# Kernel optimization log

Hardware: AMD Instinct MI355X
Metric: run time of the kernel (lower is better)

## Reference

```python
import jax, jax.numpy as jnp
import numpy as np

B, S, D, H, F, V = 64, 100, 1024, 16, 4096, 32000
DEPTH = D // H
EPS = 1e-6


def _positional_encoding(seq_len, dim):
    pos = np.arange(seq_len).reshape(seq_len, 1).astype(np.float64)
    i = np.arange(dim)
    div_term = np.power(10000.0, 2 * (i // 2) / dim)
    pe = np.zeros((seq_len, dim))
    pe[:, 0::2] = np.sin(pos / div_term[0::2])
    pe[:, 1::2] = np.cos(pos / div_term[1::2])
    return jnp.asarray(pe, dtype=jnp.float32)


def _layer_norm(x, gamma, beta):
    mean = jnp.mean(x, axis=-1, keepdims=True)
    var = jnp.mean(jnp.square(x - mean), axis=-1, keepdims=True)
    return gamma * ((x - mean) / jnp.sqrt(var + EPS)) + beta


def setup_inputs() -> dict:
    key = jax.random.key(0)
    ks = jax.random.split(key, 16)
    sd = 0.02
    inp = {
        "tokens": jax.random.randint(ks[0], (B, S), 0, V, dtype=jnp.int32),
        "emb_table": jax.random.normal(ks[1], (V, D), jnp.float32) * sd,
        "Wq": jax.random.normal(ks[2], (H, D, DEPTH), jnp.float32) * sd,
        "bq": jnp.zeros((H, DEPTH), jnp.float32),
        "Wk": jax.random.normal(ks[3], (H, D, DEPTH), jnp.float32) * sd,
        "bk": jnp.zeros((H, DEPTH), jnp.float32),
        "Wv": jax.random.normal(ks[4], (H, D, DEPTH), jnp.float32) * sd,
        "bv": jnp.zeros((H, DEPTH), jnp.float32),
        "Wo": jax.random.normal(ks[5], (D, D), jnp.float32) * sd,
        "bo": jnp.zeros((D,), jnp.float32),
        "W1": jax.random.normal(ks[6], (D, F), jnp.float32) * sd,
        "b1": jnp.zeros((F,), jnp.float32),
        "W2": jax.random.normal(ks[7], (F, D), jnp.float32) * sd,
        "b2": jnp.zeros((D,), jnp.float32),
        "gamma1": jnp.ones((D,), jnp.float32),
        "beta1": jnp.zeros((D,), jnp.float32),
        "gamma2": jnp.ones((D,), jnp.float32),
        "beta2": jnp.zeros((D,), jnp.float32),
    }
    return inp


def reference(tokens, emb_table, Wq, bq, Wk, bk, Wv, bv, Wo, bo,
              W1, b1, W2, b2, gamma1, beta1, gamma2, beta2):
    pe = _positional_encoding(S, D)  # [S, D]
    x = emb_table[tokens] + pe  # [B, S, D]

    # per-head projections (equivalent to the H separate Dense layers, stacked)
    q = jnp.einsum("bsd,hde->bhse", x, Wq) + bq[None, :, None, :]
    k = jnp.einsum("bsd,hde->bhse", x, Wk) + bk[None, :, None, :]
    v = jnp.einsum("bsd,hde->bhse", x, Wv) + bv[None, :, None, :]

    scores = jnp.einsum("bhqe,bhke->bhqk", q, k) / jnp.sqrt(jnp.float32(DEPTH))
    attn = jax.nn.softmax(scores, axis=-1)  # no mask (mask=False in Encoder)
    ctx = jnp.einsum("bhqk,bhke->bhqe", attn, v)  # [B, H, S, depth]
    # concat heads along last dim (head i -> columns i*depth:(i+1)*depth)
    ctx = jnp.transpose(ctx, (0, 2, 1, 3)).reshape(B, S, D)
    att_out = ctx @ Wo + bo

    # dropout is identity (training=False)
    x1 = _layer_norm(att_out + x, gamma1, beta1)
    ff = jax.nn.relu(x1 @ W1 + b1) @ W2 + b2
    out = _layer_norm(ff + x1, gamma2, beta2)
    return out
```

## Files before the change

kernel.cpp:

```cpp
#include <hip/hip_runtime.h>
#include <hip/hip_bf16.h>
#include <math.h>

typedef __hip_bfloat16 bf16;
typedef __attribute__((ext_vector_type(8))) short short8;
typedef __attribute__((ext_vector_type(4))) float f32x4;

static constexpr int kB = 64;
static constexpr int kS = 100;
static constexpr int kD = 1024;
static constexpr int kH = 16;
static constexpr int kF = 4096;
static constexpr int kRows = kB * kS;

__device__ __forceinline__ void gload_lds16(const void* g, void* l) {
    __builtin_amdgcn_global_load_lds(
        (const __attribute__((address_space(1))) void*)g,
        (__attribute__((address_space(3))) void*)l, 16, 0, 0);
}

union BF4 { bf16 b[4]; uint2 u; };

__global__ void pe_kernel(float* __restrict__ pe) {
    int idx = blockIdx.x * 256 + threadIdx.x;
    if (idx >= kS * kD) return;
    int s = idx / kD, i = idx % kD;
    double dt = pow(10000.0, (double)(2 * (i / 2)) / (double)kD);
    double a  = (double)s / dt;
    pe[idx] = (float)((i & 1) ? cos(a) : sin(a));
}

__global__ __launch_bounds__(256) void embed_kernel(
    const int* __restrict__ tokens, const float* __restrict__ emb,
    const float* __restrict__ pe, float* __restrict__ xf, bf16* __restrict__ xb) {
    int row = blockIdx.x, t = threadIdx.x;
    int tok = tokens[row];
    const float4* ev = (const float4*)(emb + (size_t)tok * kD);
    const float4* pv = (const float4*)(pe + (size_t)(row % kS) * kD);
    float4 a = ev[t], b = pv[t];
    float4 v; v.x = a.x + b.x; v.y = a.y + b.y; v.z = a.z + b.z; v.w = a.w + b.w;
    ((float4*)(xf + (size_t)row * kD))[t] = v;
    BF4 p; p.b[0] = __float2bfloat16(v.x); p.b[1] = __float2bfloat16(v.y);
    p.b[2] = __float2bfloat16(v.z); p.b[3] = __float2bfloat16(v.w);
    *(uint2*)(xb + (size_t)row * kD + t * 4) = p.u;
}

__global__ __launch_bounds__(256) void transpose_to_bf16(
    const float* __restrict__ in, bf16* __restrict__ out, int K, int N) {
    __shared__ float tile[64][65];
    size_t zoff = (size_t)blockIdx.z * K * N;
    int k0 = blockIdx.y * 64, n0 = blockIdx.x * 64;
    int t = threadIdx.x, r = t >> 6, c = t & 63;
#pragma unroll
    for (int it = 0; it < 16; ++it)
        tile[it * 4 + r][c] = in[zoff + (size_t)(k0 + it * 4 + r) * N + n0 + c];
    __syncthreads();
#pragma unroll
    for (int it = 0; it < 16; ++it)
        out[zoff + (size_t)(n0 + it * 4 + r) * K + k0 + c] =
            __float2bfloat16(tile[c][it * 4 + r]);
}

__global__ void concat_bias(const float* __restrict__ bq, const float* __restrict__ bk,
                            const float* __restrict__ bv, float* __restrict__ out) {
    int id = blockIdx.x * 256 + threadIdx.x;
    if (id >= 3 * kD) return;
    const float* src = (id < kD) ? bq : (id < 2 * kD) ? bk : bv;
    out[id] = src[id & (kD - 1)];
}

template <bool RELU, bool OUT_BF16>
__global__ __launch_bounds__(256) void gemm_kernel(
    const bf16* __restrict__ A, const bf16* __restrict__ Bt,
    const float* __restrict__ bias, float* __restrict__ Cf, bf16* __restrict__ Cb,
    int M, int N, int K) {
    __shared__ bf16 As[128 * 32];
    __shared__ bf16 Bs[128 * 32];
    const int t = threadIdx.x;
    const int lane = t & 63, wave = t >> 6;
    const int wr = wave >> 1, wc = wave & 1;
    const int m0 = blockIdx.y * 128, n0 = blockIdx.x * 128;

    f32x4 acc[4][4] = {};

    const int srow = t >> 2;
    const int scol = (t & 3) * 8;
    const bf16* gA = A + (size_t)(m0 + srow) * K + scol;
    const bf16* gB = Bt + (size_t)(n0 + srow) * K + scol;
    char* lA = (char*)As + t * 16;
    char* lB = (char*)Bs + t * 16;

    const int fr = lane & 15;
    const int koff = (lane >> 4) * 8;

    for (int k0 = 0; k0 < K; k0 += 32) {
        __syncthreads();
        gload_lds16(gA, lA);
        gload_lds16(gA + (size_t)64 * K, lA + 4096);
        gload_lds16(gB, lB);
        gload_lds16(gB + (size_t)64 * K, lB + 4096);
        gA += 32; gB += 32;
        __syncthreads();

        short8 fa[4], fb[4];
#pragma unroll
        for (int i = 0; i < 4; ++i) {
            fa[i] = *(const short8*)(As + (wr * 64 + i * 16 + fr) * 32 + koff);
            fb[i] = *(const short8*)(Bs + (wc * 64 + i * 16 + fr) * 32 + koff);
        }
#pragma unroll
        for (int i = 0; i < 4; ++i)
#pragma unroll
            for (int j = 0; j < 4; ++j)
                acc[i][j] = __builtin_amdgcn_mfma_f32_16x16x32_bf16(
                    fa[i], fb[j], acc[i][j], 0, 0, 0);
    }

    const int cr = (lane >> 4) * 4;
    const int cc = lane & 15;
#pragma unroll
    for (int i = 0; i < 4; ++i)
#pragma unroll
        for (int j = 0; j < 4; ++j) {
            int col = n0 + wc * 64 + j * 16 + cc;
            float bv = bias[col];
#pragma unroll
            for (int r = 0; r < 4; ++r) {
                int row = m0 + wr * 64 + i * 16 + cr + r;
                float v = acc[i][j][r] + bv;
                if (RELU) v = fmaxf(v, 0.f);
                if (OUT_BF16) Cb[(size_t)row * N + col] = __float2bfloat16(v);
                else          Cf[(size_t)row * N + col] = v;
            }
        }
}

__global__ __launch_bounds__(256) void attn_mfma_kernel(
    const bf16* __restrict__ qkvb, bf16* __restrict__ ctx) {
    __shared__ bf16 Ks[112 * 64];
    __shared__ bf16 Vt[64 * 128];
    __shared__ bf16 Ps[128 * 128];
    const int b = blockIdx.x >> 4, h = blockIdx.x & 15;
    const int t = threadIdx.x, lane = t & 63, w = t >> 6;
    const int fr = lane & 15, qq = lane >> 4;
    const size_t rbase = (size_t)b * kS * 3072 + (size_t)h * 64;

    for (int i = t; i < 64 * 14; i += 256) {
        int e = i / 14, kk = 100 + (i % 14) * 2;
        *(unsigned*)((char*)Vt + e * 256 + ((kk * 2) ^ ((e & 7) << 4))) = 0u;
    }
    for (int i = t; i < 128 * 8; i += 256) {
        int r = i / 8, c = 112 + (i % 8) * 2;
        *(unsigned*)((char*)Ps + r * 256 + ((c * 2) ^ ((r & 7) << 4))) = 0u;
    }
    for (int it = 0; it < 4; ++it) {
        int s = it * 32 + (t >> 3);
        if (s < kS) {
            int e0 = (t & 7) * 8;
            const bf16* kr = qkvb + rbase + (size_t)s * 3072 + 1024 + e0;
            short8 kv = *(const short8*)kr;
            *(short8*)((char*)Ks + s * 128 + ((e0 * 2) ^ ((s & 7) << 4))) = kv;
            short8 vv = *(const short8*)(kr + 1024);
#pragma unroll
            for (int i2 = 0; i2 < 8; ++i2) {
                int e = e0 + i2;
                *(unsigned short*)((char*)Vt + e * 256 + ((s * 2) ^ ((e & 7) << 4))) =
                    ((unsigned short*)&vv)[i2];
            }
        }
    }
    short8 qa[2][2];
#pragma unroll
    for (int rt = 0; rt < 2; ++rt)
#pragma unroll
        for (int ks = 0; ks < 2; ++ks) {
            int q = 32 * w + 16 * rt + fr; q = q < kS ? q : kS - 1;
            qa[rt][ks] = *(const short8*)(qkvb + rbase + (size_t)q * 3072 + 32 * ks + 8 * qq);
        }
    __syncthreads();

    short8 kb[7][2];
#pragma unroll
    for (int j = 0; j < 7; ++j)
#pragma unroll
        for (int ks = 0; ks < 2; ++ks)
            kb[j][ks] = *(const short8*)((char*)Ks + (16 * j + fr) * 128 +
                                         ((64 * ks + 16 * qq) ^ ((fr & 7) << 4)));

    f32x4 sc[2][7] = {};
#pragma unroll
    for (int rt = 0; rt < 2; ++rt)
#pragma unroll
        for (int j = 0; j < 7; ++j)
#pragma unroll
            for (int ks = 0; ks < 2; ++ks)
                sc[rt][j] = __builtin_amdgcn_mfma_f32_16x16x32_bf16(
                    qa[rt][ks], kb[j][ks], sc[rt][j], 0, 0, 0);

    float inv_l[2][4];
#pragma unroll
    for (int rt = 0; rt < 2; ++rt)
#pragma unroll
        for (int r = 0; r < 4; ++r) {
            float v[7];
#pragma unroll
            for (int j = 0; j < 7; ++j) v[j] = sc[rt][j][r] * 0.125f;
            if (fr >= 4) v[6] = -INFINITY;
            float m = v[0];
#pragma unroll
            for (int j = 1; j < 7; ++j) m = fmaxf(m, v[j]);
#pragma unroll
            for (int off = 8; off; off >>= 1) m = fmaxf(m, __shfl_xor(m, off));
            int row = 32 * w + 16 * rt + qq * 4 + r;
            float s = 0.f;
#pragma unroll
            for (int j = 0; j < 7; ++j) {
                float p = __expf(v[j] - m);
                s += p;
                *(bf16*)((char*)Ps + row * 256 + (((16 * j + fr) * 2) ^ ((row & 7) << 4))) =
                    __float2bfloat16(p);
            }
#pragma unroll
            for (int off = 8; off; off >>= 1) s += __shfl_xor(s, off);
            inv_l[rt][r] = 1.f / s;
        }
    __syncthreads();

    short8 pa[2][4];
#pragma unroll
    for (int rt = 0; rt < 2; ++rt)
#pragma unroll
        for (int ks = 0; ks < 4; ++ks) {
            int row = 32 * w + 16 * rt + fr;
            pa[rt][ks] = *(const short8*)((char*)Ps + row * 256 +
                                          ((64 * ks + 16 * qq) ^ ((fr & 7) << 4)));
        }
#pragma unroll
    for (int e = 0; e < 4; ++e) {
        short8 vb[4];
#pragma unroll
        for (int ks = 0; ks < 4; ++ks)
            vb[ks] = *(const short8*)((char*)Vt + (16 * e + fr) * 256 +
                                      ((64 * ks + 16 * qq) ^ ((fr & 7) << 4)));
#pragma unroll
        for (int rt = 0; rt < 2; ++rt) {
            f32x4 o = {};
#pragma unroll
            for (int ks = 0; ks < 4; ++ks)
                o = __builtin_amdgcn_mfma_f32_16x16x32_bf16(pa[rt][ks], vb[ks], o, 0, 0, 0);
#pragma unroll
            for (int r = 0; r < 4; ++r) {
                int q = 32 * w + 16 * rt + qq * 4 + r;
                if (q < kS)
                    ctx[((size_t)b * kS + q) * kD + h * 64 + 16 * e + fr] =
                        __float2bfloat16(o[r] * inv_l[rt][r]);
            }
        }
    }
}

__global__ __launch_bounds__(256) void add_ln_kernel(
    const float* __restrict__ a, const float* __restrict__ r,
    const float* __restrict__ gamma, const float* __restrict__ beta,
    float* __restrict__ outf, bf16* __restrict__ outb) {
    __shared__ float red[10];
    int row = blockIdx.x, t = threadIdx.x, lane = t & 63, w = t >> 6;
    const float4 va = ((const float4*)(a + (size_t)row * kD))[t];
    const float4 vr = ((const float4*)(r + (size_t)row * kD))[t];
    float4 x; x.x = va.x + vr.x; x.y = va.y + vr.y; x.z = va.z + vr.z; x.w = va.w + vr.w;
    float s  = x.x + x.y + x.z + x.w;
    float ss = x.x * x.x + x.y * x.y + x.z * x.z + x.w * x.w;
#pragma unroll
    for (int off = 32; off; off >>= 1) {
        s += __shfl_xor(s, off); ss += __shfl_xor(ss, off);
    }
    if (lane == 0) { red[w] = s; red[4 + w] = ss; }
    __syncthreads();
    if (t == 0) {
        float S = red[0] + red[1] + red[2] + red[3];
        float Q = red[4] + red[5] + red[6] + red[7];
        float mean = S / kD;
        float var  = Q / kD - mean * mean;
        red[8] = mean; red[9] = rsqrtf(var + 1e-6f);
    }
    __syncthreads();
    float mean = red[8], rstd = red[9];
    const float4 g  = ((const float4*)gamma)[t];
    const float4 be = ((const float4*)beta)[t];
    float4 o;
    o.x = g.x * ((x.x - mean) * rstd) + be.x;
    o.y = g.y * ((x.y - mean) * rstd) + be.y;
    o.z = g.z * ((x.z - mean) * rstd) + be.z;
    o.w = g.w * ((x.w - mean) * rstd) + be.w;
    ((float4*)(outf + (size_t)row * kD))[t] = o;
    if (outb) {
        BF4 p; p.b[0] = __float2bfloat16(o.x); p.b[1] = __float2bfloat16(o.y);
        p.b[2] = __float2bfloat16(o.z); p.b[3] = __float2bfloat16(o.w);
        *(uint2*)(outb + (size_t)row * kD + t * 4) = p.u;
    }
}

extern "C" void kernel_launch(void* const* d_in, const int* in_sizes, int n_in,
                              void* d_out, int out_size, void* d_ws, size_t ws_size,
                              hipStream_t stream) {
    const int*   tokens = (const int*)d_in[0];
    const float* emb    = (const float*)d_in[1];
    const float* Wq     = (const float*)d_in[2];
    const float* bq     = (const float*)d_in[3];
    const float* Wk     = (const float*)d_in[4];
    const float* bk     = (const float*)d_in[5];
    const float* Wv     = (const float*)d_in[6];
    const float* bv     = (const float*)d_in[7];
    const float* Wo     = (const float*)d_in[8];
    const float* bo     = (const float*)d_in[9];
    const float* W1     = (const float*)d_in[10];
    const float* b1     = (const float*)d_in[11];
    const float* W2     = (const float*)d_in[12];
    const float* b2     = (const float*)d_in[13];
    const float* g1     = (const float*)d_in[14];
    const float* be1    = (const float*)d_in[15];
    const float* g2     = (const float*)d_in[16];
    const float* be2    = (const float*)d_in[17];

    char* ws = (char*)d_ws;
    float* xf     = (float*)(ws + 0);
    bf16*  xb     = (bf16*) (ws + 26214400);
    bf16*  qkvb   = (bf16*) (ws + 39321600);
    bf16*  hbuf   = (bf16*) (ws + 0);
    float* attout = (float*)(ws + 78643200);
    float* ff     = (float*)(ws + 78643200);
    float* x1f    = (float*)(ws + 104857600);
    bf16*  x1b    = (bf16*) (ws + 131072000);
    float* pe     = (float*)(ws + 144179200);
    bf16*  wqkvt  = (bf16*) (ws + 144588800);
    bf16*  wot    = (bf16*) (ws + 150880256);
    bf16*  w1t    = (bf16*) (ws + 152977408);
    bf16*  w2t    = (bf16*) (ws + 161366016);
    float* bqkv   = (float*)(ws + 169754624);

    pe_kernel<<<400, 256, 0, stream>>>(pe);
    embed_kernel<<<kRows, 256, 0, stream>>>(tokens, emb, pe, xf, xb);

    transpose_to_bf16<<<dim3(1, 16, 16), 256, 0, stream>>>(Wq, wqkvt,               1024, 64);
    transpose_to_bf16<<<dim3(1, 16, 16), 256, 0, stream>>>(Wk, wqkvt + 1024 * 1024, 1024, 64);
    transpose_to_bf16<<<dim3(1, 16, 16), 256, 0, stream>>>(Wv, wqkvt + 2048 * 1024, 1024, 64);
    transpose_to_bf16<<<dim3(16, 16, 1), 256, 0, stream>>>(Wo, wot, 1024, 1024);
    transpose_to_bf16<<<dim3(64, 16, 1), 256, 0, stream>>>(W1, w1t, 1024, 4096);
    transpose_to_bf16<<<dim3(16, 64, 1), 256, 0, stream>>>(W2, w2t, 4096, 1024);
    concat_bias<<<12, 256, 0, stream>>>(bq, bk, bv, bqkv);

    gemm_kernel<false, true><<<dim3(24, 50), 256, 0, stream>>>(
        xb, wqkvt, bqkv, nullptr, qkvb, kRows, 3072, 1024);
    attn_mfma_kernel<<<kB * kH, 256, 0, stream>>>(qkvb, xb);
    gemm_kernel<false, false><<<dim3(8, 50), 256, 0, stream>>>(
        xb, wot, bo, attout, nullptr, kRows, 1024, 1024);
    add_ln_kernel<<<kRows, 256, 0, stream>>>(attout, xf, g1, be1, x1f, x1b);
    gemm_kernel<true, true><<<dim3(32, 50), 256, 0, stream>>>(
        x1b, w1t, b1, nullptr, hbuf, kRows, 4096, 1024);
    gemm_kernel<false, false><<<dim3(8, 50), 256, 0, stream>>>(
        hbuf, w2t, b2, ff, nullptr, kRows, 1024, 4096);
    add_ln_kernel<<<kRows, 256, 0, stream>>>(ff, x1f, g2, be2, (float*)d_out, nullptr);
}
```

Baseline: 565.3 us.

## Double-buffer GEMM LDS, swizzle block order, split-K W2 GEMM, fuse prep kernels

```diff
diff --git a/kernel.cpp b/kernel.cpp
--- a/kernel.cpp
+++ b/kernel.cpp
@@ -21,13 +21,50 @@
 
 union BF4 { bf16 b[4]; uint2 u; };
 
-__global__ void pe_kernel(float* __restrict__ pe) {
-    int idx = blockIdx.x * 256 + threadIdx.x;
-    if (idx >= kS * kD) return;
-    int s = idx / kD, i = idx % kD;
-    double dt = pow(10000.0, (double)(2 * (i / 2)) / (double)kD);
-    double a  = (double)s / dt;
-    pe[idx] = (float)((i & 1) ? cos(a) : sin(a));
+__global__ __launch_bounds__(256) void prep_kernel(
+    const float* __restrict__ Wq, const float* __restrict__ Wk,
+    const float* __restrict__ Wv, const float* __restrict__ Wo,
+    const float* __restrict__ W1, const float* __restrict__ W2,
+    const float* __restrict__ bq, const float* __restrict__ bk,
+    const float* __restrict__ bv,
+    bf16* __restrict__ wqkvt, bf16* __restrict__ wot,
+    bf16* __restrict__ w1t, bf16* __restrict__ w2t,
+    float* __restrict__ bqkv, float* __restrict__ pe) {
+    const int tb = blockIdx.x, t = threadIdx.x;
+    if (tb < 3072) {
+        __shared__ float tile[64][65];
+        const float* src; bf16* dst; int N, ldd, tid;
+        if (tb < 768) {
+            int wsel = tb / 256, rem = tb % 256, h = rem >> 4;
+            tid = rem & 15;
+            src = (wsel == 0 ? Wq : wsel == 1 ? Wk : Wv) + (size_t)h * 65536;
+            dst = wqkvt + (size_t)wsel * 1024 * 1024 + (size_t)h * 65536;
+            N = 64; ldd = 1024;
+        } else if (tb < 1024) { tid = tb - 768;  src = Wo; dst = wot; N = 1024; ldd = 1024; }
+        else if (tb < 2048)   { tid = tb - 1024; src = W1; dst = w1t; N = 4096; ldd = 1024; }
+        else                  { tid = tb - 2048; src = W2; dst = w2t; N = 1024; ldd = 4096; }
+        const int ntx = N >> 6;
+        const int k0 = (tid / ntx) * 64, n0 = (tid % ntx) * 64;
+        const int r = t >> 6, c = t & 63;
+#pragma unroll
+        for (int it = 0; it < 16; ++it)
+            tile[it * 4 + r][c] = src[(size_t)(k0 + it * 4 + r) * N + n0 + c];
+        __syncthreads();
+#pragma unroll
+        for (int it = 0; it < 16; ++it)
+            dst[(size_t)(n0 + it * 4 + r) * ldd + k0 + c] =
+                __float2bfloat16(tile[c][it * 4 + r]);
+    } else if (tb < 3084) {
+        int id = (tb - 3072) * 256 + t;
+        const float* src = (id < kD) ? bq : (id < 2 * kD) ? bk : bv;
+        bqkv[id] = src[id & (kD - 1)];
+    } else {
+        int idx = (tb - 3084) * 256 + t;
+        int s = idx / kD, i = idx % kD;
+        double dt = pow(10000.0, (double)(2 * (i / 2)) / (double)kD);
+        double a  = (double)s / dt;
+        pe[idx] = (float)((i & 1) ? cos(a) : sin(a));
+    }
 }
 
 __global__ __launch_bounds__(256) void embed_kernel(
@@ -45,77 +82,74 @@
     *(uint2*)(xb + (size_t)row * kD + t * 4) = p.u;
 }
 
-__global__ __launch_bounds__(256) void transpose_to_bf16(
-    const float* __restrict__ in, bf16* __restrict__ out, int K, int N) {
-    __shared__ float tile[64][65];
-    size_t zoff = (size_t)blockIdx.z * K * N;
-    int k0 = blockIdx.y * 64, n0 = blockIdx.x * 64;
-    int t = threadIdx.x, r = t >> 6, c = t & 63;
-#pragma unroll
-    for (int it = 0; it < 16; ++it)
-        tile[it * 4 + r][c] = in[zoff + (size_t)(k0 + it * 4 + r) * N + n0 + c];
-    __syncthreads();
-#pragma unroll
-    for (int it = 0; it < 16; ++it)
-        out[zoff + (size_t)(n0 + it * 4 + r) * K + k0 + c] =
-            __float2bfloat16(tile[c][it * 4 + r]);
-}
-
-__global__ void concat_bias(const float* __restrict__ bq, const float* __restrict__ bk,
-                            const float* __restrict__ bv, float* __restrict__ out) {
-    int id = blockIdx.x * 256 + threadIdx.x;
-    if (id >= 3 * kD) return;
-    const float* src = (id < kD) ? bq : (id < 2 * kD) ? bk : bv;
-    out[id] = src[id & (kD - 1)];
-}
+#define GEMM_COMPUTE(BUF)                                                        \
+    do {                                                                         \
+        short8 fa[4], fb[4];                                                     \
+        _Pragma("unroll") for (int i = 0; i < 4; ++i) {                          \
+            fa[i] = *(const short8*)(As[BUF] + (wr * 64 + i * 16 + fr) * 32 + koff); \
+            fb[i] = *(const short8*)(Bs[BUF] + (wc * 64 + i * 16 + fr) * 32 + koff); \
+        }                                                                        \
+        _Pragma("unroll") for (int i = 0; i < 4; ++i)                            \
+            _Pragma("unroll") for (int j = 0; j < 4; ++j)                        \
+                acc[i][j] = __builtin_amdgcn_mfma_f32_16x16x32_bf16(             \
+                    fa[i], fb[j], acc[i][j], 0, 0, 0);                           \
+    } while (0)
 
 template <bool RELU, bool OUT_BF16>
 __global__ __launch_bounds__(256) void gemm_kernel(
     const bf16* __restrict__ A, const bf16* __restrict__ Bt,
     const float* __restrict__ bias, float* __restrict__ Cf, bf16* __restrict__ Cb,
-    int M, int N, int K) {
-    __shared__ bf16 As[128 * 32];
-    __shared__ bf16 Bs[128 * 32];
+    int M, int N, int Kfull, int Kslice) {
+    __shared__ bf16 As[2][128 * 32];
+    __shared__ bf16 Bs[2][128 * 32];
     const int t = threadIdx.x;
     const int lane = t & 63, wave = t >> 6;
     const int wr = wave >> 1, wc = wave & 1;
-    const int m0 = blockIdx.y * 128, n0 = blockIdx.x * 128;
+
+    const int nx = gridDim.x, ny = gridDim.y;
+    const int lin = blockIdx.y * nx + blockIdx.x;
+    const int per = (nx * ny) >> 3;
+    const int wg  = (lin & 7) * per + (lin >> 3);
+    const int cg  = wg & 7;
+    const int t2  = wg >> 3;
+    const int by  = t2 % ny, gx = t2 / ny;
+    const int m0 = by * 128, n0 = (gx * 8 + cg) * 128;
+
+    const int kz = blockIdx.z;
+    const bf16* Az = A  + (size_t)kz * Kslice;
+    const bf16* Bz = Bt + (size_t)kz * Kslice;
 
     f32x4 acc[4][4] = {};
 
     const int srow = t >> 2;
     const int scol = (t & 3) * 8;
-    const bf16* gA = A + (size_t)(m0 + srow) * K + scol;
-    const bf16* gB = Bt + (size_t)(n0 + srow) * K + scol;
-    char* lA = (char*)As + t * 16;
-    char* lB = (char*)Bs + t * 16;
+    const bf16* gA = Az + (size_t)(m0 + srow) * Kfull + scol;
+    const bf16* gB = Bz + (size_t)(n0 + srow) * Kfull + scol;
 
     const int fr = lane & 15;
     const int koff = (lane >> 4) * 8;
 
-    for (int k0 = 0; k0 < K; k0 += 32) {
+    gload_lds16(gA,                        (char*)As[0] + t * 16);
+    gload_lds16(gA + (size_t)64 * Kfull,   (char*)As[0] + 4096 + t * 16);
+    gload_lds16(gB,                        (char*)Bs[0] + t * 16);
+    gload_lds16(gB + (size_t)64 * Kfull,   (char*)Bs[0] + 4096 + t * 16);
+    __syncthreads();
+
+    int cur = 0;
+    for (int k0 = 32; k0 < Kslice; k0 += 32) {
+        gA += 32; gB += 32;
+        const int nxt = cur ^ 1;
+        gload_lds16(gA,                      (char*)As[nxt] + t * 16);
+        gload_lds16(gA + (size_t)64 * Kfull, (char*)As[nxt] + 4096 + t * 16);
+        gload_lds16(gB,                      (char*)Bs[nxt] + t * 16);
+        gload_lds16(gB + (size_t)64 * Kfull, (char*)Bs[nxt] + 4096 + t * 16);
+        GEMM_COMPUTE(cur);
         __syncthreads();
-        gload_lds16(gA, lA);
-        gload_lds16(gA + (size_t)64 * K, lA + 4096);
-        gload_lds16(gB, lB);
-        gload_lds16(gB + (size_t)64 * K, lB + 4096);
-        gA += 32; gB += 32;
-        __syncthreads();
-
-        short8 fa[4], fb[4];
-#pragma unroll
-        for (int i = 0; i < 4; ++i) {
-            fa[i] = *(const short8*)(As + (wr * 64 + i * 16 + fr) * 32 + koff);
-            fb[i] = *(const short8*)(Bs + (wc * 64 + i * 16 + fr) * 32 + koff);
-        }
-#pragma unroll
-        for (int i = 0; i < 4; ++i)
-#pragma unroll
-            for (int j = 0; j < 4; ++j)
-                acc[i][j] = __builtin_amdgcn_mfma_f32_16x16x32_bf16(
-                    fa[i], fb[j], acc[i][j], 0, 0, 0);
-    }
-
+        cur = nxt;
+    }
+    GEMM_COMPUTE(cur);
+
+    if (Cf) Cf += (size_t)kz * M * N;
     const int cr = (lane >> 4) * 4;
     const int cc = lane & 15;
 #pragma unroll
@@ -123,7 +157,7 @@
 #pragma unroll
         for (int j = 0; j < 4; ++j) {
             int col = n0 + wc * 64 + j * 16 + cc;
-            float bv = bias[col];
+            float bv = (kz == 0) ? bias[col] : 0.f;
 #pragma unroll
             for (int r = 0; r < 4; ++r) {
                 int row = m0 + wr * 64 + i * 16 + cr + r;
@@ -260,7 +294,8 @@
 }
 
 __global__ __launch_bounds__(256) void add_ln_kernel(
-    const float* __restrict__ a, const float* __restrict__ r,
+    const float* __restrict__ a, const float* __restrict__ a2,
+    const float* __restrict__ r,
     const float* __restrict__ gamma, const float* __restrict__ beta,
     float* __restrict__ outf, bf16* __restrict__ outb) {
     __shared__ float red[10];
@@ -268,6 +303,10 @@
     const float4 va = ((const float4*)(a + (size_t)row * kD))[t];
     const float4 vr = ((const float4*)(r + (size_t)row * kD))[t];
     float4 x; x.x = va.x + vr.x; x.y = va.y + vr.y; x.z = va.z + vr.z; x.w = va.w + vr.w;
+    if (a2) {
+        const float4 v2 = ((const float4*)(a2 + (size_t)row * kD))[t];
+        x.x += v2.x; x.y += v2.y; x.z += v2.z; x.w += v2.w;
+    }
     float s  = x.x + x.y + x.z + x.w;
     float ss = x.x * x.x + x.y * x.y + x.z * x.z + x.w * x.w;
 #pragma unroll
@@ -327,8 +366,8 @@
     bf16*  xb     = (bf16*) (ws + 26214400);
     bf16*  qkvb   = (bf16*) (ws + 39321600);
     bf16*  hbuf   = (bf16*) (ws + 0);
+    float* ffp    = (float*)(ws + 52428800);
     float* attout = (float*)(ws + 78643200);
-    float* ff     = (float*)(ws + 78643200);
     float* x1f    = (float*)(ws + 104857600);
     bf16*  x1b    = (bf16*) (ws + 131072000);
     float* pe     = (float*)(ws + 144179200);
@@ -338,26 +377,20 @@
     bf16*  w2t    = (bf16*) (ws + 161366016);
     float* bqkv   = (float*)(ws + 169754624);
 
-    pe_kernel<<<400, 256, 0, stream>>>(pe);
+    prep_kernel<<<3484, 256, 0, stream>>>(Wq, Wk, Wv, Wo, W1, W2, bq, bk, bv,
+                                          wqkvt, wot, w1t, w2t, bqkv, pe);
     embed_kernel<<<kRows, 256, 0, stream>>>(tokens, emb, pe, xf, xb);
 
-    transpose_to_bf16<<<dim3(1, 16, 16), 256, 0, stream>>>(Wq, wqkvt,               1024, 64);
-    transpose_to_bf16<<<dim3(1, 16, 16), 256, 0, stream>>>(Wk, wqkvt + 1024 * 1024, 1024, 64);
-    transpose_to_bf16<<<dim3(1, 16, 16), 256, 0, stream>>>(Wv, wqkvt + 2048 * 1024, 1024, 64);
-    transpose_to_bf16<<<dim3(16, 16, 1), 256, 0, stream>>>(Wo, wot, 1024, 1024);
-    transpose_to_bf16<<<dim3(64, 16, 1), 256, 0, stream>>>(W1, w1t, 1024, 4096);
-    transpose_to_bf16<<<dim3(16, 64, 1), 256, 0, stream>>>(W2, w2t, 4096, 1024);
-    concat_bias<<<12, 256, 0, stream>>>(bq, bk, bv, bqkv);
-
-    gemm_kernel<false, true><<<dim3(24, 50), 256, 0, stream>>>(
-        xb, wqkvt, bqkv, nullptr, qkvb, kRows, 3072, 1024);
+    gemm_kernel<false, true><<<dim3(24, 50, 1), 256, 0, stream>>>(
+        xb, wqkvt, bqkv, nullptr, qkvb, kRows, 3072, 1024, 1024);
     attn_mfma_kernel<<<kB * kH, 256, 0, stream>>>(qkvb, xb);
-    gemm_kernel<false, false><<<dim3(8, 50), 256, 0, stream>>>(
-        xb, wot, bo, attout, nullptr, kRows, 1024, 1024);
-    add_ln_kernel<<<kRows, 256, 0, stream>>>(attout, xf, g1, be1, x1f, x1b);
-    gemm_kernel<true, true><<<dim3(32, 50), 256, 0, stream>>>(
-        x1b, w1t, b1, nullptr, hbuf, kRows, 4096, 1024);
-    gemm_kernel<false, false><<<dim3(8, 50), 256, 0, stream>>>(
-        hbuf, w2t, b2, ff, nullptr, kRows, 1024, 4096);
-    add_ln_kernel<<<kRows, 256, 0, stream>>>(ff, x1f, g2, be2, (float*)d_out, nullptr);
-}
+    gemm_kernel<false, false><<<dim3(8, 50, 1), 256, 0, stream>>>(
+        xb, wot, bo, attout, nullptr, kRows, 1024, 1024, 1024);
+    add_ln_kernel<<<kRows, 256, 0, stream>>>(attout, nullptr, xf, g1, be1, x1f, x1b);
+    gemm_kernel<true, true><<<dim3(32, 50, 1), 256, 0, stream>>>(
+        x1b, w1t, b1, nullptr, hbuf, kRows, 4096, 1024, 1024);
+    gemm_kernel<false, false><<<dim3(8, 50, 2), 256, 0, stream>>>(
+        hbuf, w2t, b2, ffp, nullptr, kRows, 1024, 4096, 2048);
+    add_ln_kernel<<<kRows, 256, 0, stream>>>(ffp, ffp + (size_t)kRows * kD, x1f,
+                                             g2, be2, (float*)d_out, nullptr);
+}
```

After: 529.7 us. -6.3%, faster.
